# Optimization experiments

Hardware: AMD Instinct MI355X
Metric: run time of the kernel (lower is better)

The kernel has to match this reference:

```python
import jax, jax.numpy as jnp
import numpy as np

N = 2048   # nodes
B = 8      # batch
T = 4      # input time steps
C = 64     # channels
H = 2      # num_heads
E_RAND = 8192
NEG_SLOPE = 0.2
EPS = 1e-5


def setup_inputs() -> dict:
    key = jax.random.key(0)
    ks = jax.random.split(key, 26)
    s = 0.05
    x = jax.random.normal(ks[0], (B, N, T, C), jnp.float32)
    src_r = jax.random.randint(ks[1], (E_RAND,), 0, N)
    dst_r = jax.random.randint(ks[2], (E_RAND,), 0, N)
    loop = jnp.arange(N)
    src = jnp.concatenate([src_r, loop])  # self loops guarantee in-degree >= 1
    dst = jnp.concatenate([dst_r, loop])
    p = {}
    # two GATConv layers: fc weight (C, H*C), attn_l/attn_r (H, C), bias (H*C)
    p['W1'] = jax.random.normal(ks[3], (C, H * C), jnp.float32) * s
    p['al1'] = jax.random.normal(ks[4], (H, C), jnp.float32) * s
    p['ar1'] = jax.random.normal(ks[5], (H, C), jnp.float32) * s
    p['b1'] = jnp.zeros((H * C,), jnp.float32)
    p['W2'] = jax.random.normal(ks[6], (C, H * C), jnp.float32) * s
    p['al2'] = jax.random.normal(ks[7], (H, C), jnp.float32) * s
    p['ar2'] = jax.random.normal(ks[8], (H, C), jnp.float32) * s
    p['b2'] = jnp.zeros((H * C,), jnp.float32)
    # LayerNorm([n, c]) params for the two 'N' layers
    p['ln1_w'] = jnp.ones((N, C), jnp.float32)
    p['ln1_b'] = jnp.zeros((N, C), jnp.float32)
    p['ln2_w'] = jnp.ones((N, C), jnp.float32)
    p['ln2_b'] = jnp.zeros((N, C), jnp.float32)
    # OutputLayer: tconv1 kernel (1, (H-1)*T+1)=(1,5), ln, tconv2 (1,1), fc(C*12 -> 12)
    KT = (H - 1) * T + 1
    p['tc1_w'] = jax.random.normal(ks[9], (C, C, 1, KT), jnp.float32) * s
    p['tc1_b'] = jnp.zeros((C,), jnp.float32)
    p['ln3_w'] = jnp.ones((N, C), jnp.float32)
    p['ln3_b'] = jnp.zeros((N, C), jnp.float32)
    p['tc2_w'] = jax.random.normal(ks[10], (C, C, 1, 1), jnp.float32) * s
    p['tc2_b'] = jnp.zeros((C,), jnp.float32)
    p['fc_w'] = jax.random.normal(ks[11], (12, C * 12), jnp.float32) * s
    p['fc_b'] = jnp.zeros((12,), jnp.float32)
    return dict(x=x, src=src, dst=dst, **p)


def _gat_layer(x, src, dst, W, al, ar, bias):
    # x: [B, N, t, C] -> GATConv over N nodes, features [B, t, C] per node (eval: no dropout)
    b, n, t, c = x.shape
    h = jnp.transpose(x, (1, 0, 2, 3))                     # [N, B, t, C]
    feat = jnp.einsum('nbtc,cd->nbtd', h, W).reshape(n, b, t, H, c)
    el = jnp.einsum('nbthc,hc->nbth', feat, al)            # [N, B, t, H]
    er = jnp.einsum('nbthc,hc->nbth', feat, ar)
    e = jax.nn.leaky_relu(el[src] + er[dst], NEG_SLOPE)    # [E, B, t, H]
    m = jax.ops.segment_max(e, dst, num_segments=n)
    a = jnp.exp(e - m[dst])
    ssum = jax.ops.segment_sum(a, dst, num_segments=n)
    alpha = a / ssum[dst]                                  # edge softmax over in-edges
    out = jax.ops.segment_sum(feat[src] * alpha[..., None], dst, num_segments=n)
    out = out + bias.reshape(1, 1, 1, H, c)                # [N, B, t, H, C]
    out = out.reshape(n, b, t * H, c)
    return jax.nn.relu(jnp.transpose(out, (1, 0, 2, 3)))   # [B, N, t*H, C]


def _ln_nc(x, w, b):
    # x: [..., N, C]; normalize jointly over last two dims like nn.LayerNorm([n, c])
    mu = x.mean(axis=(-2, -1), keepdims=True)
    var = x.var(axis=(-2, -1), keepdims=True)
    return (x - mu) / jnp.sqrt(var + EPS) * w + b


def _conv2d(x, w, b):
    y = jax.lax.conv_general_dilated(x, w, (1, 1), 'VALID',
                                     dimension_numbers=('NCHW', 'OIHW', 'NCHW'))
    return y + b.reshape(1, -1, 1, 1)


def reference(x, src, dst, W1, al1, ar1, b1, ln1_w, ln1_b,
              W2, al2, ar2, b2, ln2_w, ln2_b,
              tc1_w, tc1_b, ln3_w, ln3_b, tc2_w, tc2_b, fc_w, fc_b):
    # S
    x = _gat_layer(x, src, dst, W1, al1, ar1, b1)          # [B,N,T*H,C]
    # N : LN([n,c]) applied on permuted [B,t,N,C]
    x = jnp.transpose(_ln_nc(jnp.transpose(x, (0, 2, 1, 3)), ln1_w, ln1_b), (0, 2, 1, 3))
    # S
    x = _gat_layer(x, src, dst, W2, al2, ar2, b2)          # [B,N,T*H*H,C]
    # N
    x = jnp.transpose(_ln_nc(jnp.transpose(x, (0, 2, 1, 3)), ln2_w, ln2_b), (0, 2, 1, 3))
    # OutputLayer
    b, n, t, c = x.shape
    xp = jnp.transpose(x, (0, 3, 1, 2))                    # [B,C,N,t]
    x_t1 = _conv2d(xp, tc1_w, tc1_b)                       # [B,C,N,12]
    x_ln = _ln_nc(jnp.transpose(x_t1, (0, 3, 2, 1)), ln3_w, ln3_b)  # [B,12,N,C]
    x_t2 = _conv2d(jnp.transpose(x_ln, (0, 3, 2, 1)), tc2_w, tc2_b)  # [B,C,N,12]
    # faithful to torch: direct reshape of [B,C,N,12] into (B, N, C*12)
    flat = jnp.reshape(x_t2, (b, n, c * 12))
    return flat @ fc_w.T + fc_b                            # [B,N,12]
```

## Files before the change

### kernel.cpp

```cpp
#include <hip/hip_runtime.h>
#include <math.h>

#define NN 2048
#define BB 8
#define HH 2
#define NEG 0.2f
#define EPSL 1e-5f

typedef short bf16x8 __attribute__((ext_vector_type(8)));
typedef float f32x4 __attribute__((ext_vector_type(4)));

__device__ __forceinline__ float wave_reduce_sum(float v){
#pragma unroll
  for (int m = 32; m > 0; m >>= 1) v += __shfl_xor(v, m, 64);
  return v;
}

__device__ __forceinline__ unsigned short f2b(float f){
  union { float f; unsigned u; } v; v.f = f;
  unsigned r = v.u + 0x7FFFu + ((v.u >> 16) & 1u);
  return (unsigned short)(r >> 16);
}
__device__ __forceinline__ float b2f(unsigned short u){
  union { unsigned u; float f; } v; v.u = ((unsigned)u) << 16; return v.f;
}

__global__ void k_count(const int* __restrict__ dst, int E, int* cnt){
  int i = blockIdx.x*256+threadIdx.x; if(i<E) atomicAdd(&cnt[dst[i]],1);
}

__global__ void k_scan(const int* __restrict__ cnt, int* row_start, int* cursor){
  __shared__ int part[256];
  int tid = threadIdx.x;
  int loc[8]; int s = 0;
#pragma unroll
  for(int j=0;j<8;j++){ loc[j]=s; s += cnt[tid*8+j]; }
  part[tid]=s; __syncthreads();
  for(int off=1; off<256; off<<=1){
    int v = (tid>=off)? part[tid-off] : 0;
    __syncthreads();
    part[tid] += v;
    __syncthreads();
  }
  int excl = (tid==0)? 0 : part[tid-1];
#pragma unroll
  for(int j=0;j<8;j++){ int v=excl+loc[j]; row_start[tid*8+j]=v; cursor[tid*8+j]=v; }
  if(tid==255) row_start[2048]=excl+s;
}

__global__ void k_fill(const int* __restrict__ dst, const int* __restrict__ src,
                       int E, int* cursor, int* csrsrc){
  int i = blockIdx.x*256+threadIdx.x;
  if(i<E){ int p = atomicAdd(&cursor[dst[i]],1); csrsrc[p]=src[i]; }
}

__global__ void k_prep(const float* __restrict__ W1, const float* __restrict__ al1, const float* __restrict__ ar1,
                       const float* __restrict__ W2, const float* __restrict__ al2, const float* __restrict__ ar2,
                       const float* __restrict__ tc1w, const float* __restrict__ tc2w,
                       const float* __restrict__ fcw,
                       unsigned short* wf1, unsigned short* wf2,
                       unsigned short* wc1, unsigned short* wc2,
                       unsigned short* wfc, int* counts){
  int blk = blockIdx.x; int tid = threadIdx.x;
  if(blk==0){ for(int i=tid;i<8192;i+=256){ int k=i>>7, co=i&127; wf1[co*72+k]=f2b(W1[i]); } }
  else if(blk==1){ for(int i=tid;i<8192;i+=256){ int k=i>>7, co=i&127; wf2[co*72+k]=f2b(W2[i]); } }
  else if(blk==2){
    int k=tid>>2, q=tid&3, h=q&1;
    { const float* av=(q>>1)?ar1:al1; float s=0.f;
      for(int c=0;c<64;c++) s+=W1[k*128+h*64+c]*av[h*64+c];
      wf1[(128+q)*72+k]=f2b(s); }
    { const float* av=(q>>1)?ar2:al2; float s=0.f;
      for(int c=0;c<64;c++) s+=W2[k*128+h*64+c]*av[h*64+c];
      wf2[(128+q)*72+k]=f2b(s); }
  }
  else if(blk==3){
    for(int co=0;co<64;co++)
      for(int kap=tid;kap<320;kap+=256){
        int kt=kap>>6, ci=kap&63;
        wc1[co*320+kap]=f2b(tc1w[(co*64+ci)*5+kt]);
      }
  }
  else if(blk==4){ for(int i=tid;i<4096;i+=256) wc2[i]=f2b(tc2w[i]); }
  else if(blk==5){
    for(int i=tid;i<12288;i+=256){
      int o=i/768, f=i%768;
      wfc[i] = (o<12)? f2b(fcw[o*768+f]) : (unsigned short)0;
    }
  }
  else { for(int i=tid;i<2048;i+=256) counts[i]=0; }
}

__global__ __launch_bounds__(256) void k_prepx1(
  const float* __restrict__ x, const unsigned short* __restrict__ wf,
  unsigned short* __restrict__ xg, float* __restrict__ el, float* __restrict__ er)
{
  __shared__ __align__(16) unsigned short xs[64*72];
  int tid = threadIdx.x; int r0 = blockIdx.x*64;
  for(int idx=tid; idx<1024; idx+=256){
    int rl=idx>>4, c4=(idx&15)*4;
    int row=r0+rl; int n_=row>>5, rb=row&31, t=rb>>3, b=rb&7;
    float4 v = *(const float4*)&x[(((size_t)b*2048+n_)*4 + t)*64 + c4];
    unsigned p0 = (unsigned)f2b(v.x) | ((unsigned)f2b(v.y)<<16);
    unsigned p1 = (unsigned)f2b(v.z) | ((unsigned)f2b(v.w)<<16);
    uint2 u = make_uint2(p0,p1);
    *(uint2*)&xs[rl*72+c4] = u;
    *(uint2*)&xg[(size_t)row*64 + c4] = u;
  }
  __syncthreads();
  int wv=tid>>6, lane=tid&63, lhi=lane>>4, llo=lane&15;
  f32x4 accE = (f32x4){0.f,0.f,0.f,0.f};
#pragma unroll
  for(int s=0;s<2;s++){
    bf16x8 a = *(const bf16x8*)&xs[(wv*16+llo)*72 + s*32 + lhi*8];
    bf16x8 be = *(const bf16x8*)&wf[(128+llo)*72 + s*32 + lhi*8];
    accE = __builtin_amdgcn_mfma_f32_16x16x32_bf16(a, be, accE, 0,0,0);
  }
  if(llo<4){
#pragma unroll
    for(int i=0;i<4;i++){
      int row = r0 + wv*16 + lhi*4 + i; int n_=row>>5, rb=row&31;
      int idx = n_*64 + rb*2 + (llo&1);
      if(llo<2) el[idx]=accE[i]; else er[idx]=accE[i];
    }
  }
}

__global__ __launch_bounds__(256) void k_prepx2(
  const unsigned short* __restrict__ x1g, const float* __restrict__ mu,
  const float* __restrict__ inv, const float* __restrict__ lnw, const float* __restrict__ lnb,
  const unsigned short* __restrict__ wf,
  unsigned short* __restrict__ xg2, float* __restrict__ el, float* __restrict__ er)
{
  __shared__ __align__(16) unsigned short xs[64*72];
  int n = blockIdx.x; int tid = threadIdx.x;
  for(int idx=tid; idx<1024; idx+=256){
    int rl=idx>>4, c4=(idx&15)*4;
    int t2=rl>>3, b=rl&7; int g=b*8+t2;
    uint2 u = *(const uint2*)&x1g[((size_t)n*64 + rl)*64 + c4];
    float m_=mu[g], iv=inv[g];
    float4 w4 = *(const float4*)&lnw[n*64+c4];
    float4 b4 = *(const float4*)&lnb[n*64+c4];
    float v0=(b2f((unsigned short)(u.x&0xffff))-m_)*iv*w4.x+b4.x;
    float v1=(b2f((unsigned short)(u.x>>16))  -m_)*iv*w4.y+b4.y;
    float v2=(b2f((unsigned short)(u.y&0xffff))-m_)*iv*w4.z+b4.z;
    float v3=(b2f((unsigned short)(u.y>>16))  -m_)*iv*w4.w+b4.w;
    unsigned p0 = (unsigned)f2b(v0)|((unsigned)f2b(v1)<<16);
    unsigned p1 = (unsigned)f2b(v2)|((unsigned)f2b(v3)<<16);
    uint2 o = make_uint2(p0,p1);
    *(uint2*)&xs[rl*72+c4] = o;
    *(uint2*)&xg2[((size_t)n*64+rl)*64 + c4] = o;
  }
  __syncthreads();
  int wv=tid>>6, lane=tid&63, lhi=lane>>4, llo=lane&15;
  f32x4 accE=(f32x4){0.f,0.f,0.f,0.f};
#pragma unroll
  for(int s=0;s<2;s++){
    bf16x8 a = *(const bf16x8*)&xs[(wv*16+llo)*72 + s*32 + lhi*8];
    bf16x8 be = *(const bf16x8*)&wf[(128+llo)*72 + s*32 + lhi*8];
    accE = __builtin_amdgcn_mfma_f32_16x16x32_bf16(a, be, accE, 0,0,0);
  }
  if(llo<4){
#pragma unroll
    for(int i=0;i<4;i++){
      int rb = wv*16 + lhi*4 + i;
      int idx = n*128 + rb*2 + (llo&1);
      if(llo<2) el[idx]=accE[i]; else er[idx]=accE[i];
    }
  }
}

template<int IR>
__global__ __launch_bounds__(256) void k_gat_fused(
  const unsigned short* __restrict__ xg, const float* __restrict__ el,
  const float* __restrict__ er, const int* __restrict__ row_start,
  const int* __restrict__ csrsrc, const unsigned short* __restrict__ wf,
  const float* __restrict__ bias, unsigned short* __restrict__ out,
  float2* __restrict__ pg)
{
  constexpr int TPR = 256/IR;
  constexpr int CPL = 64/TPR;
  constexpr int NU  = CPL/8;
  constexpr int RT2 = IR/32;
  __shared__ __align__(16) unsigned short aggl[2][IR][72];
  int n = blockIdx.x; int tid = threadIdx.x;
  int beg = row_start[n]; int deg = row_start[n+1]-beg;
  int wv = tid>>6, lane = tid&63, lhi = lane>>4, llo = lane&15;
  int hW = wv>>1;

  bf16x8 Bf[4][2];
#pragma unroll
  for(int ct=0;ct<4;ct++)
#pragma unroll
    for(int s=0;s<2;s++)
      Bf[ct][s] = *(const bf16x8*)&wf[(hW*64+ct*16+llo)*72 + s*32 + lhi*8];

  int r = tid/TPR; int dbase = (tid%TPR)*CPL;
  float2 ern = *(const float2*)&er[(size_t)n*(2*IR) + r*2];
  float acc0[CPL], acc1[CPL];
#pragma unroll
  for(int i=0;i<CPL;i++){ acc0[i]=0.f; acc1[i]=0.f; }
  float ss0=0.f, ss1=0.f;
  const unsigned short* xb = xg + (size_t)r*64 + dbase;

  int sn = csrsrc[beg];
  float2 elv = *(const float2*)&el[(size_t)sn*(2*IR) + r*2];
  uint4 cur[NU];
  {
    const unsigned short* fp = xb + (size_t)sn*(IR*64);
#pragma unroll
    for(int u=0;u<NU;u++) cur[u] = *(const uint4*)(fp + u*8);
  }
  for(int j=0;j<deg;j++){
    float2 elv2 = make_float2(0.f,0.f); uint4 nxt[NU];
    if(j+1<deg){
      int sn2 = csrsrc[beg+j+1];
      elv2 = *(const float2*)&el[(size_t)sn2*(2*IR) + r*2];
      const unsigned short* fp2 = xb + (size_t)sn2*(IR*64);
#pragma unroll
      for(int u=0;u<NU;u++) nxt[u] = *(const uint4*)(fp2 + u*8);
    }
    float e0 = elv.x + ern.x; e0 = e0>0.f? e0 : NEG*e0;
    float e1 = elv.y + ern.y; e1 = e1>0.f? e1 : NEG*e1;
    float w0 = __expf(e0), w1 = __expf(e1);
    ss0 += w0; ss1 += w1;
    const unsigned short* pu = (const unsigned short*)cur;
#pragma unroll
    for(int i=0;i<CPL;i++){ float xv = b2f(pu[i]); acc0[i] += w0*xv; acc1[i] += w1*xv; }
    if(j+1<deg){
      elv = elv2;
#pragma unroll
      for(int u=0;u<NU;u++) cur[u] = nxt[u];
    }
  }
  float is0 = 1.f/ss0, is1 = 1.f/ss1;
#pragma unroll
  for(int i=0;i<CPL;i++){
    aggl[0][r][dbase+i] = f2b(acc0[i]*is0);
    aggl[1][r][dbase+i] = f2b(acc1[i]*is1);
  }
  __syncthreads();

  f32x4 acc[RT2][4];
#pragma unroll
  for(int rt=0;rt<RT2;rt++)
#pragma unroll
    for(int ct=0;ct<4;ct++) acc[rt][ct]=(f32x4){0.f,0.f,0.f,0.f};
  int rbase = (wv&1)*(IR/2);
#pragma unroll
  for(int rt=0;rt<RT2;rt++){
#pragma unroll
    for(int s=0;s<2;s++){
      bf16x8 a = *(const bf16x8*)&aggl[hW][rbase+rt*16+llo][s*32+lhi*8];
#pragma unroll
      for(int ct=0;ct<4;ct++)
        acc[rt][ct] = __builtin_amdgcn_mfma_f32_16x16x32_bf16(a, Bf[ct][s], acc[rt][ct], 0,0,0);
    }
  }

#pragma unroll
  for(int rt=0;rt<RT2;rt++){
    float bb[4];
#pragma unroll
    for(int ct=0;ct<4;ct++) bb[ct] = bias[hW*64 + ct*16 + llo];
#pragma unroll
    for(int i=0;i<4;i++){
      int ro = rbase + rt*16 + lhi*4 + i;
      int t_new = (ro>>3)*2 + hW; int bq = ro&7;
      size_t off;
      if constexpr (IR==32) off = ((size_t)n*64 + t_new*8 + bq)*64;
      else                  off = (((size_t)bq*2048 + n)*16 + t_new)*64;
      float ps=0.f, pq=0.f;
#pragma unroll
      for(int ct=0;ct<4;ct++){
        float v = fmaxf(acc[rt][ct][i] + bb[ct], 0.f);
        out[off + ct*16 + llo] = f2b(v);
        ps += v; pq += v*v;
      }
#pragma unroll
      for(int mM=1;mM<=8;mM<<=1){ ps += __shfl_xor(ps,mM,64); pq += __shfl_xor(pq,mM,64); }
      if(llo==0) pg[(size_t)(ro*2+hW)*2048 + n] = make_float2(ps,pq);
    }
  }
}

__global__ void k_lnfin(const float2* __restrict__ p, float* __restrict__ mu, float* __restrict__ inv,
                        int mode, int TT2){
  int g = blockIdx.x; int tid = threadIdx.x;
  float s=0.f, q=0.f;
  if(mode==0){
    int base = g*2048;
    for(int i=tid;i<2048;i+=256){ float2 v = p[base + i]; s+=v.x; q+=v.y; }
  } else {
    int b = g/12; int to = g - b*12;
    for(int i=tid;i<8192;i+=256){
      int n_ = i>>2; int wv = i&3;
      float2 v = p[((size_t)(b*2048+n_)*12 + to)*4 + wv];
      s+=v.x; q+=v.y;
    }
  }
  s = wave_reduce_sum(s); q = wave_reduce_sum(q);
  __shared__ float red[8];
  int wid=tid>>6, lane=tid&63;
  if(lane==0){ red[wid]=s; red[4+wid]=q; }
  __syncthreads();
  if(tid==0){
    float S=red[0]+red[1]+red[2]+red[3];
    float Q=red[4]+red[5]+red[6]+red[7];
    float cnt = 131072.f;
    float m = S/cnt; float var = Q/cnt - m*m;
    int gout;
    if(mode==0){ int h=g&1; int b=(g>>1)&7; int t=g>>4; gout = b*TT2 + t*2 + h; }
    else gout = g;
    mu[gout]=m; inv[gout]=rsqrtf(var+EPSL);
  }
}

template<int TIN, int TOUT, int KT, bool PSUM>
__global__ __launch_bounds__(256,4) void k_convT(
  const unsigned short* __restrict__ xin,
  const float* __restrict__ mu, const float* __restrict__ inv,
  const float* __restrict__ lnw, const float* __restrict__ lnb,
  const unsigned short* __restrict__ wcg,
  const float* __restrict__ bias,
  unsigned short* __restrict__ y, float2* __restrict__ pr4)
{
  constexpr int K = KT*64;
  constexpr int KSTEPS = K/32;
  constexpr int XPAD = 72;
  constexpr int XN = TIN*XPAD + 8;
  constexpr int NODES = 16;
  constexpr int RT = NODES*TOUT/16;
  __shared__ __align__(16) unsigned short xs[NODES*XN];
  int tid = threadIdx.x;
  int bn0 = blockIdx.x*NODES;
  int r0 = bn0*TOUT;
  int wv_ = tid>>6, lane = tid&63, lhi = lane>>4, llo = lane&15;

  bf16x8 bB[KSTEPS];
  {
    const unsigned short* wrow = wcg + (wv_*16+llo)*K;
#pragma unroll
    for(int s=0;s<KSTEPS;s++) bB[s] = *(const bf16x8*)(wrow + s*32 + lhi*8);
  }

  {
    int nd = tid>>4; int c4 = (tid&15)*4;
    int bn = bn0+nd; int b = bn0>>11; int n_ = bn&2047;
    float4 w4 = *(const float4*)&lnw[n_*64+c4];
    float4 b4 = *(const float4*)&lnb[n_*64+c4];
    const unsigned short* xp = xin + (size_t)bn*TIN*64 + c4;
    unsigned short* p0 = &xs[nd*XN + c4];
#pragma unroll
    for(int t=0;t<TIN;t++){
      uint2 u = *(const uint2*)(xp + t*64);
      float m_ = mu[b*TIN+t], iv = inv[b*TIN+t];
      float iw0 = iv*w4.x, iw1 = iv*w4.y, iw2 = iv*w4.z, iw3 = iv*w4.w;
      unsigned short* p = p0 + t*XPAD;
      p[0]=f2b((b2f((unsigned short)(u.x&0xffff))-m_)*iw0+b4.x);
      p[1]=f2b((b2f((unsigned short)(u.x>>16))  -m_)*iw1+b4.y);
      p[2]=f2b((b2f((unsigned short)(u.y&0xffff))-m_)*iw2+b4.z);
      p[3]=f2b((b2f((unsigned short)(u.y>>16))  -m_)*iw3+b4.w);
    }
  }
  __syncthreads();

  f32x4 acc[RT];
#pragma unroll
  for(int rt=0;rt<RT;rt++) acc[rt] = (f32x4){0.f,0.f,0.f,0.f};

#pragma unroll
  for(int rt=0; rt<RT; rt++){
    int rr = rt*16 + llo;
    int nd = rr/TOUT; int to = rr - nd*TOUT;
    const unsigned short* ap = &xs[nd*XN + to*XPAD];
#pragma unroll
    for(int s=0;s<KSTEPS;s++){
      int ktap = s>>1; int cib = ((s&1)<<5) + lhi*8;
      bf16x8 a = *(const bf16x8*)(ap + ktap*XPAD + cib);
      acc[rt] = __builtin_amdgcn_mfma_f32_16x16x32_bf16(a, bB[s], acc[rt], 0,0,0);
    }
  }

  float bb = bias[wv_*16 + llo];
#pragma unroll
  for(int rt=0; rt<RT; rt++){
    float vs[4];
#pragma unroll
    for(int i=0;i<4;i++) vs[i] = acc[rt][i] + bb;
#pragma unroll
    for(int i=0;i<4;i++)
      y[(size_t)(r0 + rt*16 + lhi*4 + i)*64 + wv_*16 + llo] = f2b(vs[i]);
    if constexpr (PSUM){
#pragma unroll
      for(int i=0;i<4;i++){
        float s = vs[i], q = vs[i]*vs[i];
#pragma unroll
        for(int mM=1;mM<=8;mM<<=1){ s += __shfl_xor(s,mM,64); q += __shfl_xor(q,mM,64); }
        if(llo==0) pr4[(size_t)(r0 + rt*16 + lhi*4 + i)*4 + wv_] = make_float2(s,q);
      }
    }
  }
}

__global__ __launch_bounds__(256) void k_fcm(const unsigned short* __restrict__ xt2,
  const unsigned short* __restrict__ wfc, const float* __restrict__ fb, float* __restrict__ out)
{
  constexpr int APAD = 102;
  __shared__ unsigned short A[2][64*APAD];
  int tid = threadIdx.x;
  int b = blockIdx.x>>5, nh = blockIdx.x&31;
  int wv = tid>>6, lane = tid&63, lhi = lane>>4, llo = lane&15;

  bf16x8 Bp[24];
  {
    const unsigned short* wrow = wfc + llo*768 + lhi*8;
#pragma unroll
    for(int s=0;s<24;s++) Bp[s] = *(const bf16x8*)(wrow + s*32);
  }

  int it_col[3], it_c8[3];
#pragma unroll
  for(int j=0;j<3;j++){
    int idx = j*256 + tid;
    it_c8[j] = idx&7;
    int tau = (idx>>3)%12; int nl = idx/96;
    it_col[j] = nl*12 + tau;
  }
  const unsigned short* xbase = xt2 + (size_t)(b*2048 + nh*64)*768;

  uint4 r[3];
#pragma unroll
  for(int j=0;j<3;j++)
    r[j] = *(const uint4*)(xbase + (size_t)it_col[j]*64 + it_c8[j]*8);
#pragma unroll
  for(int j=0;j<3;j++){
    const unsigned short* pr = (const unsigned short*)&r[j];
#pragma unroll
    for(int i=0;i<8;i++) A[0][(it_c8[j]*8+i)*APAD + it_col[j]] = pr[i];
  }
  __syncthreads();

  f32x4 acc = (f32x4){0.f,0.f,0.f,0.f};
  for(int ch=0; ch<8; ch++){
    int cur = ch&1;
    if(ch<7){
      const unsigned short* nb = xbase + (size_t)(ch+1)*8*768;
#pragma unroll
      for(int j=0;j<3;j++)
        r[j] = *(const uint4*)(nb + (size_t)it_col[j]*64 + it_c8[j]*8);
    }
#pragma unroll
    for(int s=0;s<3;s++){
      bf16x8 a = *(const bf16x8*)&A[cur][(wv*16+llo)*APAD + s*32 + lhi*8];
      acc = __builtin_amdgcn_mfma_f32_16x16x32_bf16(a, Bp[ch*3+s], acc, 0,0,0);
    }
    if(ch<7){
#pragma unroll
      for(int j=0;j<3;j++){
        const unsigned short* pr = (const unsigned short*)&r[j];
#pragma unroll
        for(int i=0;i<8;i++) A[cur^1][(it_c8[j]*8+i)*APAD + it_col[j]] = pr[i];
      }
      __syncthreads();
    }
  }

  if(llo<12){
    float bbv = fb[llo];
#pragma unroll
    for(int i=0;i<4;i++){
      int c = wv*16 + lhi*4 + i;
      out[((size_t)b*2048 + c*32 + nh)*12 + llo] = acc[i] + bbv;
    }
  }
}

extern "C" void kernel_launch(void* const* d_in, const int* in_sizes, int n_in,
                              void* d_out, int out_size, void* d_ws, size_t ws_size,
                              hipStream_t stream) {
  (void)n_in; (void)out_size; (void)ws_size;
  const float* x    = (const float*)d_in[0];
  const int*   src  = (const int*)d_in[1];
  const int*   dst  = (const int*)d_in[2];
  const float* W1   = (const float*)d_in[3];
  const float* al1  = (const float*)d_in[4];
  const float* ar1  = (const float*)d_in[5];
  const float* b1   = (const float*)d_in[6];
  const float* W2   = (const float*)d_in[7];
  const float* al2  = (const float*)d_in[8];
  const float* ar2  = (const float*)d_in[9];
  const float* b2   = (const float*)d_in[10];
  const float* ln1w = (const float*)d_in[11];
  const float* ln1b = (const float*)d_in[12];
  const float* ln2w = (const float*)d_in[13];
  const float* ln2b = (const float*)d_in[14];
  const float* tc1w = (const float*)d_in[15];
  const float* tc1b = (const float*)d_in[16];
  const float* ln3w = (const float*)d_in[17];
  const float* ln3b = (const float*)d_in[18];
  const float* tc2w = (const float*)d_in[19];
  const float* tc2b = (const float*)d_in[20];
  const float* fcw  = (const float*)d_in[21];
  const float* fcb  = (const float*)d_in[22];
  int E = in_sizes[1];

  unsigned short* U = (unsigned short*)d_ws;
  unsigned short* xg1 = U + 0;
  unsigned short* x1g = U + 4194304;
  unsigned short* xg2 = U + 12582912;
  unsigned short* x2  = U + 20971520;
  unsigned short* xt1 = U + 0;
  unsigned short* xt2 = U + 12582912;
  unsigned short* wf1 = U + 37748736;
  unsigned short* wf2 = wf1 + 10368;
  unsigned short* wc1 = wf2 + 10368;
  unsigned short* wc2 = wc1 + 20480;
  unsigned short* wfc = wc2 + 4096;
  float* F = (float*)(wfc + 12288);
  float* el1 = F;
  float* er1 = el1 + 131072;
  float* el2 = er1 + 131072;
  float* er2 = el2 + 262144;
  float2* pg1 = (float2*)(er2 + 262144);
  float2* pg2 = pg1 + 131072;
  float2* pr4 = pg2 + 262144;
  float* mu1  = (float*)(pr4 + 786432);
  float* inv1 = mu1 + 64;
  float* mu2  = inv1 + 64;
  float* inv2 = mu2 + 128;
  float* mu3  = inv2 + 128;
  float* inv3 = mu3 + 96;
  int* counts = (int*)(inv3 + 96);
  int* cursor = counts + 2048;
  int* rs     = cursor + 2048;
  int* csrsrc = rs + 2049;

  int eb = (E+255)/256;

  k_prep<<<7,256,0,stream>>>(W1,al1,ar1, W2,al2,ar2, tc1w, tc2w, fcw, wf1, wf2, wc1, wc2, wfc, counts);
  k_count<<<eb,256,0,stream>>>(dst, E, counts);
  k_scan<<<1,256,0,stream>>>(counts, rs, cursor);
  k_fill<<<eb,256,0,stream>>>(dst, src, E, cursor, csrsrc);

  k_prepx1<<<1024,256,0,stream>>>(x, wf1, xg1, el1, er1);
  k_gat_fused<32><<<2048,256,0,stream>>>(xg1, el1, er1, rs, csrsrc, wf1, b1, x1g, pg1);
  k_lnfin<<<64,256,0,stream>>>(pg1, mu1, inv1, 0, 8);

  k_prepx2<<<2048,256,0,stream>>>(x1g, mu1, inv1, ln1w, ln1b, wf2, xg2, el2, er2);
  k_gat_fused<64><<<2048,256,0,stream>>>(xg2, el2, er2, rs, csrsrc, wf2, b2, x2, pg2);
  k_lnfin<<<128,256,0,stream>>>(pg2, mu2, inv2, 0, 16);

  k_convT<16,12,5,true><<<1024,256,0,stream>>>(x2, mu2, inv2, ln2w, ln2b, wc1, tc1b, xt1, pr4);
  k_lnfin<<<96,256,0,stream>>>(pr4, mu3, inv3, 1, 0);

  k_convT<12,12,1,false><<<1024,256,0,stream>>>(xt1, mu3, inv3, ln3w, ln3b, wc2, tc2b, xt2, nullptr);

  k_fcm<<<256,256,0,stream>>>(xt2, wfc, fcb, (float*)d_out);
}
```

Measured before the change: 175.4 us.

## Fuse CSR count and scan into one block; retile conv MFMA for A reuse

```diff
diff --git a/kernel.cpp b/kernel.cpp
--- a/kernel.cpp
+++ b/kernel.cpp
@@ -25,13 +25,14 @@
   union { unsigned u; float f; } v; v.u = ((unsigned)u) << 16; return v.f;
 }
 
-__global__ void k_count(const int* __restrict__ dst, int E, int* cnt){
-  int i = blockIdx.x*256+threadIdx.x; if(i<E) atomicAdd(&cnt[dst[i]],1);
-}
-
-__global__ void k_scan(const int* __restrict__ cnt, int* row_start, int* cursor){
+__global__ void k_csr1(const int* __restrict__ dst, int E, int* row_start, int* cursor){
+  __shared__ int cnt[2048];
   __shared__ int part[256];
   int tid = threadIdx.x;
+  for(int i=tid;i<2048;i+=256) cnt[i]=0;
+  __syncthreads();
+  for(int i=tid;i<E;i+=256) atomicAdd(&cnt[dst[i]],1);
+  __syncthreads();
   int loc[8]; int s = 0;
 #pragma unroll
   for(int j=0;j<8;j++){ loc[j]=s; s += cnt[tid*8+j]; }
@@ -60,7 +61,7 @@
                        const float* __restrict__ fcw,
                        unsigned short* wf1, unsigned short* wf2,
                        unsigned short* wc1, unsigned short* wc2,
-                       unsigned short* wfc, int* counts){
+                       unsigned short* wfc){
   int blk = blockIdx.x; int tid = threadIdx.x;
   if(blk==0){ for(int i=tid;i<8192;i+=256){ int k=i>>7, co=i&127; wf1[co*72+k]=f2b(W1[i]); } }
   else if(blk==1){ for(int i=tid;i<8192;i+=256){ int k=i>>7, co=i&127; wf2[co*72+k]=f2b(W2[i]); } }
@@ -81,13 +82,12 @@
       }
   }
   else if(blk==4){ for(int i=tid;i<4096;i+=256) wc2[i]=f2b(tc2w[i]); }
-  else if(blk==5){
+  else {
     for(int i=tid;i<12288;i+=256){
       int o=i/768, f=i%768;
       wfc[i] = (o<12)? f2b(fcw[o*768+f]) : (unsigned short)0;
     }
   }
-  else { for(int i=tid;i<2048;i+=256) counts[i]=0; }
 }
 
 __global__ __launch_bounds__(256) void k_prepx1(
@@ -292,9 +292,9 @@
     for(int i=tid;i<2048;i+=256){ float2 v = p[base + i]; s+=v.x; q+=v.y; }
   } else {
     int b = g/12; int to = g - b*12;
-    for(int i=tid;i<8192;i+=256){
-      int n_ = i>>2; int wv = i&3;
-      float2 v = p[((size_t)(b*2048+n_)*12 + to)*4 + wv];
+    for(int i=tid;i<4096;i+=256){
+      int n_ = i>>1; int s2 = i&1;
+      float2 v = p[((size_t)(b*2048+n_)*12 + to)*2 + s2];
       s+=v.x; q+=v.y;
     }
   }
@@ -316,31 +316,34 @@
 }
 
 template<int TIN, int TOUT, int KT, bool PSUM>
-__global__ __launch_bounds__(256,4) void k_convT(
+__global__ __launch_bounds__(256) void k_convT(
   const unsigned short* __restrict__ xin,
   const float* __restrict__ mu, const float* __restrict__ inv,
   const float* __restrict__ lnw, const float* __restrict__ lnb,
   const unsigned short* __restrict__ wcg,
   const float* __restrict__ bias,
-  unsigned short* __restrict__ y, float2* __restrict__ pr4)
+  unsigned short* __restrict__ y, float2* __restrict__ pr2)
 {
   constexpr int K = KT*64;
   constexpr int KSTEPS = K/32;
   constexpr int XPAD = 72;
   constexpr int XN = TIN*XPAD + 8;
   constexpr int NODES = 16;
-  constexpr int RT = NODES*TOUT/16;
+  constexpr int HALF = NODES*TOUT/2;
+  constexpr int RT = HALF/16;
   __shared__ __align__(16) unsigned short xs[NODES*XN];
   int tid = threadIdx.x;
   int bn0 = blockIdx.x*NODES;
   int r0 = bn0*TOUT;
   int wv_ = tid>>6, lane = tid&63, lhi = lane>>4, llo = lane&15;
-
-  bf16x8 bB[KSTEPS];
-  {
-    const unsigned short* wrow = wcg + (wv_*16+llo)*K;
-#pragma unroll
-    for(int s=0;s<KSTEPS;s++) bB[s] = *(const bf16x8*)(wrow + s*32 + lhi*8);
+  int hr = wv_&1, chf = wv_>>1;
+
+  bf16x8 bB[2][KSTEPS];
+#pragma unroll
+  for(int ct=0;ct<2;ct++){
+    const unsigned short* wrow = wcg + (chf*32+ct*16+llo)*K;
+#pragma unroll
+    for(int s=0;s<KSTEPS;s++) bB[ct][s] = *(const bf16x8*)(wrow + s*32 + lhi*8);
   }
 
   {
@@ -364,39 +367,39 @@
   }
   __syncthreads();
 
-  f32x4 acc[RT];
-#pragma unroll
-  for(int rt=0;rt<RT;rt++) acc[rt] = (f32x4){0.f,0.f,0.f,0.f};
+  f32x4 acc[RT][2];
+#pragma unroll
+  for(int rt=0;rt<RT;rt++){ acc[rt][0]=(f32x4){0.f,0.f,0.f,0.f}; acc[rt][1]=(f32x4){0.f,0.f,0.f,0.f}; }
 
 #pragma unroll
   for(int rt=0; rt<RT; rt++){
-    int rr = rt*16 + llo;
+    int rr = hr*HALF + rt*16 + llo;
     int nd = rr/TOUT; int to = rr - nd*TOUT;
     const unsigned short* ap = &xs[nd*XN + to*XPAD];
 #pragma unroll
     for(int s=0;s<KSTEPS;s++){
       int ktap = s>>1; int cib = ((s&1)<<5) + lhi*8;
       bf16x8 a = *(const bf16x8*)(ap + ktap*XPAD + cib);
-      acc[rt] = __builtin_amdgcn_mfma_f32_16x16x32_bf16(a, bB[s], acc[rt], 0,0,0);
-    }
-  }
-
-  float bb = bias[wv_*16 + llo];
+      acc[rt][0] = __builtin_amdgcn_mfma_f32_16x16x32_bf16(a, bB[0][s], acc[rt][0], 0,0,0);
+      acc[rt][1] = __builtin_amdgcn_mfma_f32_16x16x32_bf16(a, bB[1][s], acc[rt][1], 0,0,0);
+    }
+  }
+
+  float bb0 = bias[chf*32 + llo], bb1 = bias[chf*32 + 16 + llo];
 #pragma unroll
   for(int rt=0; rt<RT; rt++){
-    float vs[4];
-#pragma unroll
-    for(int i=0;i<4;i++) vs[i] = acc[rt][i] + bb;
-#pragma unroll
-    for(int i=0;i<4;i++)
-      y[(size_t)(r0 + rt*16 + lhi*4 + i)*64 + wv_*16 + llo] = f2b(vs[i]);
-    if constexpr (PSUM){
-#pragma unroll
-      for(int i=0;i<4;i++){
-        float s = vs[i], q = vs[i]*vs[i];
+#pragma unroll
+    for(int i=0;i<4;i++){
+      int row = r0 + hr*HALF + rt*16 + lhi*4 + i;
+      float v0 = acc[rt][0][i] + bb0;
+      float v1 = acc[rt][1][i] + bb1;
+      y[(size_t)row*64 + chf*32 + llo]      = f2b(v0);
+      y[(size_t)row*64 + chf*32 + 16 + llo] = f2b(v1);
+      if constexpr (PSUM){
+        float s = v0+v1, q = v0*v0+v1*v1;
 #pragma unroll
         for(int mM=1;mM<=8;mM<<=1){ s += __shfl_xor(s,mM,64); q += __shfl_xor(q,mM,64); }
-        if(llo==0) pr4[(size_t)(r0 + rt*16 + lhi*4 + i)*4 + wv_] = make_float2(s,q);
+        if(llo==0) pr2[(size_t)row*2 + chf] = make_float2(s,q);
       }
     }
   }
@@ -523,23 +526,21 @@
   float* er2 = el2 + 262144;
   float2* pg1 = (float2*)(er2 + 262144);
   float2* pg2 = pg1 + 131072;
-  float2* pr4 = pg2 + 262144;
-  float* mu1  = (float*)(pr4 + 786432);
+  float2* pr2 = pg2 + 262144;
+  float* mu1  = (float*)(pr2 + 786432);
   float* inv1 = mu1 + 64;
   float* mu2  = inv1 + 64;
   float* inv2 = mu2 + 128;
   float* mu3  = inv2 + 128;
   float* inv3 = mu3 + 96;
-  int* counts = (int*)(inv3 + 96);
-  int* cursor = counts + 2048;
+  int* cursor = (int*)(inv3 + 96);
   int* rs     = cursor + 2048;
   int* csrsrc = rs + 2049;
 
   int eb = (E+255)/256;
 
-  k_prep<<<7,256,0,stream>>>(W1,al1,ar1, W2,al2,ar2, tc1w, tc2w, fcw, wf1, wf2, wc1, wc2, wfc, counts);
-  k_count<<<eb,256,0,stream>>>(dst, E, counts);
-  k_scan<<<1,256,0,stream>>>(counts, rs, cursor);
+  k_prep<<<6,256,0,stream>>>(W1,al1,ar1, W2,al2,ar2, tc1w, tc2w, fcw, wf1, wf2, wc1, wc2, wfc);
+  k_csr1<<<1,256,0,stream>>>(dst, E, rs, cursor);
   k_fill<<<eb,256,0,stream>>>(dst, src, E, cursor, csrsrc);
 
   k_prepx1<<<1024,256,0,stream>>>(x, wf1, xg1, el1, er1);
@@ -550,8 +551,8 @@
   k_gat_fused<64><<<2048,256,0,stream>>>(xg2, el2, er2, rs, csrsrc, wf2, b2, x2, pg2);
   k_lnfin<<<128,256,0,stream>>>(pg2, mu2, inv2, 0, 16);
 
-  k_convT<16,12,5,true><<<1024,256,0,stream>>>(x2, mu2, inv2, ln2w, ln2b, wc1, tc1b, xt1, pr4);
-  k_lnfin<<<96,256,0,stream>>>(pr4, mu3, inv3, 1, 0);
+  k_convT<16,12,5,true><<<1024,256,0,stream>>>(x2, mu2, inv2, ln2w, ln2b, wc1, tc1b, xt1, pr2);
+  k_lnfin<<<96,256,0,stream>>>(pr2, mu3, inv3, 1, 0);
 
   k_convT<12,12,1,false><<<1024,256,0,stream>>>(xt1, mu3, inv3, ln3w, ln3b, wc2, tc2b, xt2, nullptr);
 
```

Measured after the change: 179.3 us. 1.02x slower.

## Merge weight prep, CSR build and layer-1 projection into one setup kernel

Applied to the files above, without the earlier changes.

```diff
diff --git a/kernel.cpp b/kernel.cpp
--- a/kernel.cpp
+++ b/kernel.cpp
@@ -25,46 +25,21 @@
   union { unsigned u; float f; } v; v.u = ((unsigned)u) << 16; return v.f;
 }
 
-__global__ void k_count(const int* __restrict__ dst, int E, int* cnt){
-  int i = blockIdx.x*256+threadIdx.x; if(i<E) atomicAdd(&cnt[dst[i]],1);
-}
-
-__global__ void k_scan(const int* __restrict__ cnt, int* row_start, int* cursor){
-  __shared__ int part[256];
-  int tid = threadIdx.x;
-  int loc[8]; int s = 0;
-#pragma unroll
-  for(int j=0;j<8;j++){ loc[j]=s; s += cnt[tid*8+j]; }
-  part[tid]=s; __syncthreads();
-  for(int off=1; off<256; off<<=1){
-    int v = (tid>=off)? part[tid-off] : 0;
-    __syncthreads();
-    part[tid] += v;
-    __syncthreads();
-  }
-  int excl = (tid==0)? 0 : part[tid-1];
-#pragma unroll
-  for(int j=0;j<8;j++){ int v=excl+loc[j]; row_start[tid*8+j]=v; cursor[tid*8+j]=v; }
-  if(tid==255) row_start[2048]=excl+s;
-}
-
-__global__ void k_fill(const int* __restrict__ dst, const int* __restrict__ src,
-                       int E, int* cursor, int* csrsrc){
-  int i = blockIdx.x*256+threadIdx.x;
-  if(i<E){ int p = atomicAdd(&cursor[dst[i]],1); csrsrc[p]=src[i]; }
-}
-
-__global__ void k_prep(const float* __restrict__ W1, const float* __restrict__ al1, const float* __restrict__ ar1,
-                       const float* __restrict__ W2, const float* __restrict__ al2, const float* __restrict__ ar2,
-                       const float* __restrict__ tc1w, const float* __restrict__ tc2w,
-                       const float* __restrict__ fcw,
-                       unsigned short* wf1, unsigned short* wf2,
-                       unsigned short* wc1, unsigned short* wc2,
-                       unsigned short* wfc, int* counts){
+__global__ __launch_bounds__(256) void k_setup(
+  const int* __restrict__ dst, const int* __restrict__ src, int E,
+  const float* __restrict__ W1, const float* __restrict__ al1, const float* __restrict__ ar1,
+  const float* __restrict__ W2, const float* __restrict__ al2, const float* __restrict__ ar2,
+  const float* __restrict__ tc1w, const float* __restrict__ tc2w, const float* __restrict__ fcw,
+  const float* __restrict__ x,
+  unsigned short* wf1, unsigned short* wf2,
+  unsigned short* wc1, unsigned short* wc2, unsigned short* wfc,
+  int* row_start, int* csrsrc,
+  unsigned short* __restrict__ xg, float* __restrict__ el, float* __restrict__ er)
+{
   int blk = blockIdx.x; int tid = threadIdx.x;
-  if(blk==0){ for(int i=tid;i<8192;i+=256){ int k=i>>7, co=i&127; wf1[co*72+k]=f2b(W1[i]); } }
-  else if(blk==1){ for(int i=tid;i<8192;i+=256){ int k=i>>7, co=i&127; wf2[co*72+k]=f2b(W2[i]); } }
-  else if(blk==2){
+  if(blk==0){ for(int i=tid;i<8192;i+=256){ int k=i>>7, co=i&127; wf1[co*72+k]=f2b(W1[i]); } return; }
+  if(blk==1){ for(int i=tid;i<8192;i+=256){ int k=i>>7, co=i&127; wf2[co*72+k]=f2b(W2[i]); } return; }
+  if(blk==2){
     int k=tid>>2, q=tid&3, h=q&1;
     { const float* av=(q>>1)?ar1:al1; float s=0.f;
       for(int c=0;c<64;c++) s+=W1[k*128+h*64+c]*av[h*64+c];
@@ -72,30 +47,64 @@
     { const float* av=(q>>1)?ar2:al2; float s=0.f;
       for(int c=0;c<64;c++) s+=W2[k*128+h*64+c]*av[h*64+c];
       wf2[(128+q)*72+k]=f2b(s); }
-  }
-  else if(blk==3){
+    return;
+  }
+  if(blk==3){
     for(int co=0;co<64;co++)
       for(int kap=tid;kap<320;kap+=256){
         int kt=kap>>6, ci=kap&63;
         wc1[co*320+kap]=f2b(tc1w[(co*64+ci)*5+kt]);
       }
-  }
-  else if(blk==4){ for(int i=tid;i<4096;i+=256) wc2[i]=f2b(tc2w[i]); }
-  else if(blk==5){
+    return;
+  }
+  if(blk==4){ for(int i=tid;i<4096;i+=256) wc2[i]=f2b(tc2w[i]); return; }
+  if(blk==5){
     for(int i=tid;i<12288;i+=256){
       int o=i/768, f=i%768;
       wfc[i] = (o<12)? f2b(fcw[o*768+f]) : (unsigned short)0;
     }
-  }
-  else { for(int i=tid;i<2048;i+=256) counts[i]=0; }
-}
-
-__global__ __launch_bounds__(256) void k_prepx1(
-  const float* __restrict__ x, const unsigned short* __restrict__ wf,
-  unsigned short* __restrict__ xg, float* __restrict__ el, float* __restrict__ er)
-{
+    return;
+  }
+  if(blk==6){
+    __shared__ int cnt[2048];
+    __shared__ int part[256];
+    for(int i=tid;i<2048;i+=256) cnt[i]=0;
+    __syncthreads();
+    for(int i=tid;i<E;i+=256) atomicAdd(&cnt[dst[i]],1);
+    __syncthreads();
+    int loc[8]; int s=0;
+#pragma unroll
+    for(int j=0;j<8;j++){ loc[j]=s; s += cnt[tid*8+j]; }
+    part[tid]=s; __syncthreads();
+    for(int off=1; off<256; off<<=1){
+      int v = (tid>=off)? part[tid-off] : 0;
+      __syncthreads();
+      part[tid] += v;
+      __syncthreads();
+    }
+    int excl = (tid==0)? 0 : part[tid-1];
+#pragma unroll
+    for(int j=0;j<8;j++){ int v=excl+loc[j]; row_start[tid*8+j]=v; cnt[tid*8+j]=v; }
+    if(tid==255) row_start[2048]=excl+s;
+    __syncthreads();
+    for(int i=tid;i<E;i+=256){
+      int p = atomicAdd(&cnt[dst[i]],1);
+      csrsrc[p]=src[i];
+    }
+    return;
+  }
+
   __shared__ __align__(16) unsigned short xs[64*72];
-  int tid = threadIdx.x; int r0 = blockIdx.x*64;
+  __shared__ __align__(16) unsigned short wl[16*72];
+  int r0 = (blk-7)*64;
+  for(int i=tid;i<16*72;i+=256) wl[i]=0;
+  __syncthreads();
+  {
+    int k=tid>>2, q=tid&3, h=q&1;
+    const float* av=(q>>1)?ar1:al1; float s=0.f;
+    for(int c=0;c<64;c++) s+=W1[k*128+h*64+c]*av[h*64+c];
+    wl[q*72+k]=f2b(s);
+  }
   for(int idx=tid; idx<1024; idx+=256){
     int rl=idx>>4, c4=(idx&15)*4;
     int row=r0+rl; int n_=row>>5, rb=row&31, t=rb>>3, b=rb&7;
@@ -112,7 +121,7 @@
 #pragma unroll
   for(int s=0;s<2;s++){
     bf16x8 a = *(const bf16x8*)&xs[(wv*16+llo)*72 + s*32 + lhi*8];
-    bf16x8 be = *(const bf16x8*)&wf[(128+llo)*72 + s*32 + lhi*8];
+    bf16x8 be = *(const bf16x8*)&wl[llo*72 + s*32 + lhi*8];
     accE = __builtin_amdgcn_mfma_f32_16x16x32_bf16(a, be, accE, 0,0,0);
   }
   if(llo<4){
@@ -530,19 +539,14 @@
   float* inv2 = mu2 + 128;
   float* mu3  = inv2 + 128;
   float* inv3 = mu3 + 96;
-  int* counts = (int*)(inv3 + 96);
-  int* cursor = counts + 2048;
-  int* rs     = cursor + 2048;
+  int* rs     = (int*)(inv3 + 96);
   int* csrsrc = rs + 2049;
 
-  int eb = (E+255)/256;
-
-  k_prep<<<7,256,0,stream>>>(W1,al1,ar1, W2,al2,ar2, tc1w, tc2w, fcw, wf1, wf2, wc1, wc2, wfc, counts);
-  k_count<<<eb,256,0,stream>>>(dst, E, counts);
-  k_scan<<<1,256,0,stream>>>(counts, rs, cursor);
-  k_fill<<<eb,256,0,stream>>>(dst, src, E, cursor, csrsrc);
-
-  k_prepx1<<<1024,256,0,stream>>>(x, wf1, xg1, el1, er1);
+  k_setup<<<1031,256,0,stream>>>(dst, src, E, W1,al1,ar1, W2,al2,ar2,
+                                 tc1w, tc2w, fcw, x,
+                                 wf1, wf2, wc1, wc2, wfc, rs, csrsrc,
+                                 xg1, el1, er1);
+
   k_gat_fused<32><<<2048,256,0,stream>>>(xg1, el1, er1, rs, csrsrc, wf1, b1, x1g, pg1);
   k_lnfin<<<64,256,0,stream>>>(pg1, mu1, inv1, 0, 8);
 
```

After: 175.5 us. No clear change (+0.1%).
